# Performance work log

Hardware: AMD Instinct MI355X
Metric: run time of the kernel (lower is better)

## Reference

```python
import jax, jax.numpy as jnp
import numpy as np

C = 64      # n_feats
DG = 8      # deformable groups
K = 3       # kernel size


def _lrelu(v):
    return jnp.where(v >= 0, v, 0.1 * v)


def _conv3x3(v, w, b):
    out = jax.lax.conv_general_dilated(
        v, w, window_strides=(1, 1), padding=((1, 1), (1, 1)),
        dimension_numbers=('NCHW', 'OIHW', 'NCHW'))
    return out + b[None, :, None, None]


def _up2(v):
    # bilinear upsample x2, align_corners=True (separable gather + lerp)
    B, Cc, H, W = v.shape
    def coords(n):
        c = jnp.arange(2 * n, dtype=jnp.float32) * ((n - 1) / (2 * n - 1))
        i0 = jnp.floor(c).astype(jnp.int32)
        i1 = jnp.minimum(i0 + 1, n - 1)
        f = (c - i0).astype(v.dtype)
        return i0, i1, f
    y0, y1, fy = coords(H)
    x0, x1, fx = coords(W)
    t = v[:, :, y0, :] * (1 - fy)[None, None, :, None] + v[:, :, y1, :] * fy[None, None, :, None]
    return t[:, :, :, x0] * (1 - fx)[None, None, None, :] + t[:, :, :, x1] * fx[None, None, None, :]


def _deform_conv(x, offset, mask, w, b):
    # modulated deformable conv (DCNv2), stride=1, pad=1, dil=1
    B, Cc, H, W = x.shape
    K2 = K * K
    cpg = Cc // DG
    off_y = offset[:, :DG * K2].reshape(B, DG, K2, H, W)
    off_x = offset[:, DG * K2:].reshape(B, DG, K2, H, W)
    m = mask.reshape(B, DG, 1, K2, H, W)
    ky, kx = jnp.meshgrid(jnp.arange(K) - 1, jnp.arange(K) - 1, indexing='ij')
    ky = ky.reshape(K2).astype(x.dtype)
    kx = kx.reshape(K2).astype(x.dtype)
    # absolute sampling positions [B, DG, K2, H, W]
    py = off_y + ky[None, None, :, None, None] + jnp.arange(H, dtype=x.dtype)[None, None, None, :, None]
    px = off_x + kx[None, None, :, None, None] + jnp.arange(W, dtype=x.dtype)[None, None, None, None, :]
    y0f = jnp.floor(py)
    x0f = jnp.floor(px)
    wy = py - y0f
    wx = px - x0f
    y0 = y0f.astype(jnp.int32)
    x0 = x0f.astype(jnp.int32)
    xg = x.reshape(B, DG, cpg, H * W)
    def corner(yi, xi, wgt):
        valid = ((yi >= 0) & (yi < H) & (xi >= 0) & (xi < W)).astype(x.dtype)
        yc = jnp.clip(yi, 0, H - 1)
        xc = jnp.clip(xi, 0, W - 1)
        idx = (yc * W + xc).reshape(B, DG, 1, K2 * H * W)
        g = jnp.take_along_axis(xg, jnp.broadcast_to(idx, (B, DG, cpg, K2 * H * W)), axis=3)
        g = g.reshape(B, DG, cpg, K2, H, W)
        return g * (wgt * valid)[:, :, None]
    val = (corner(y0, x0, (1 - wy) * (1 - wx))
           + corner(y0, x0 + 1, (1 - wy) * wx)
           + corner(y0 + 1, x0, wy * (1 - wx))
           + corner(y0 + 1, x0 + 1, wy * wx))
    val = val * m
    wr = w.reshape(Cc, DG, cpg, K2)
    return jnp.einsum('bgckhw,ogck->bohw', val, wr) + b[None, :, None, None]


def setup_inputs() -> dict:
    key = jax.random.key(0)
    ks = jax.random.split(key, 18)
    B, H, W = 2, 128, 128
    def p(k, shape):
        return jax.random.normal(k, shape, jnp.float32) * 0.05
    return {
        'x': jax.random.normal(ks[0], (B, C, H, W), jnp.float32),
        'y': jax.random.normal(ks[1], (B, C, H, W), jnp.float32),
        'prev_offset': jax.random.normal(ks[2], (B, C, H // 2, W // 2), jnp.float32),
        'prev_stage_fea': jax.random.normal(ks[3], (B, C, H // 2, W // 2), jnp.float32),
        'w1': p(ks[4], (C, 2 * C, 3, 3)), 'b1': jnp.zeros((C,), jnp.float32),
        'w2': p(ks[5], (C, 2 * C, 3, 3)), 'b2': jnp.zeros((C,), jnp.float32),
        'w3': p(ks[6], (C, C, 3, 3)), 'b3': jnp.zeros((C,), jnp.float32),
        'w_off': p(ks[7], (DG * 3 * K * K, C, 3, 3)), 'b_off': jnp.zeros((DG * 3 * K * K,), jnp.float32),
        'w_dcn': p(ks[8], (C, C, 3, 3)), 'b_dcn': jnp.zeros((C,), jnp.float32),
        'w_fea': p(ks[9], (C, 2 * C, 3, 3)), 'b_fea': jnp.zeros((C,), jnp.float32),
    }


def reference(x, y, prev_offset, prev_stage_fea,
              w1, b1, w2, b2, w3, b3, w_off, b_off, w_dcn, b_dcn, w_fea, b_fea):
    prev_offset = _up2(prev_offset)
    off = _lrelu(_conv3x3(jnp.concatenate([x, y], axis=1), w1, b1))
    off = _lrelu(_conv3x3(jnp.concatenate([off, prev_offset * 2], axis=1), w2, b2))
    off = _lrelu(_conv3x3(off, w3, b3))
    # DCNv2Pack: offsets/mask predicted from the offset feature
    co = _conv3x3(off, w_off, b_off)
    o1, o2, m = jnp.split(co, 3, axis=1)
    dcn_offset = jnp.concatenate([o1, o2], axis=1)
    m = jax.nn.sigmoid(m)
    fea = _deform_conv(x, dcn_offset, m, w_dcn, b_dcn)
    prev_fea = _up2(prev_stage_fea)
    out = _lrelu(_conv3x3(jnp.concatenate([fea, prev_fea], axis=1), w_fea, b_fea))
    return (off, out)
```

## Files before the change

kernel.cpp:

```cpp
#include <hip/hip_runtime.h>
#include <math.h>

typedef __bf16 bf16x8 __attribute__((ext_vector_type(8)));
typedef float f32x4 __attribute__((ext_vector_type(4)));
typedef unsigned short u16;
typedef __attribute__((address_space(3))) unsigned int lds_u32;
typedef const __attribute__((address_space(1))) unsigned int glb_u32;

__device__ __forceinline__ u16 f2bf(float f) {
    unsigned int u = __builtin_bit_cast(unsigned int, f);
    unsigned int r = (u + 0x7FFFu + ((u >> 16) & 1u)) >> 16;
    return (u16)r;
}
__device__ __forceinline__ float bf2f(u16 u) {
    unsigned int v = ((unsigned int)u) << 16;
    return __builtin_bit_cast(float, v);
}
__device__ __forceinline__ unsigned int pack2(float a, float b) {
    return (unsigned int)f2bf(a) | ((unsigned int)f2bf(b) << 16);
}
__device__ __forceinline__ bf16x8 ld8(const u16* p) {
    uint4 u = *reinterpret_cast<const uint4*>(p);
    return __builtin_bit_cast(bf16x8, u);
}
__device__ __forceinline__ void gload_lds16(const u16* g, u16* l) {
#if __has_builtin(__builtin_amdgcn_global_load_lds)
    __builtin_amdgcn_global_load_lds((glb_u32*)g, (lds_u32*)l, 16, 0, 0);
#else
    *reinterpret_cast<uint4*>(l) = *reinterpret_cast<const uint4*>(g);
#endif
}

__device__ __forceinline__ void dev_zero(u16* base, int nimg, int C, int B, int tid) {
    int idx = B * 256 + tid;
    int c8 = C >> 3;
    int tot = nimg * 516 * c8;
    if (idx >= tot) return;
    int cb = idx % c8;
    int t = idx / c8;
    int pb = t % 516;
    int img = t / 516;
    int y, x;
    if (pb < 130)      { y = 0;        x = pb; }
    else if (pb < 260) { y = 129;      x = pb - 130; }
    else if (pb < 388) { y = pb - 259; x = 0; }
    else               { y = pb - 387; x = 129; }
    u16* d = base + ((size_t)img * 16900 + (size_t)y * 130 + x) * C + cb * 8;
    uint4 z = {0u, 0u, 0u, 0u};
    *reinterpret_cast<uint4*>(d) = z;
}

__device__ __forceinline__ void dev_repack(const float* w, u16* dst,
                                           int Cout, int Cin, int mode, int B, int tid) {
    int idx = B * 256 + tid;
    int total = Cout * Cin * 9;
    if (idx >= total) return;
    int kk = idx % 9;
    int t = idx / 9;
    int ci = t % Cin;
    int o = t / Cin;
    u16 v = f2bf(w[idx]);
    size_t d;
    if (mode == 0) d = (size_t)o * (9 * Cin) + kk * Cin + ci;
    else           d = (size_t)o * 576 + (ci >> 3) * 72 + kk * 8 + (ci & 7);
    dst[d] = v;
}

__device__ __forceinline__ void dev_to_nhwc(const float* src, u16* dst,
                                            int c0, int Ctot, int B, int tid) {
    int idx = B * 256 + tid;
    int pix = idx & 16383, b = idx >> 14;
    int y = pix >> 7, x = pix & 127;
    const float* s = src + (size_t)b * 64 * 16384 + pix;
    u16* d = dst + (((size_t)b * 16900) + (size_t)(y + 1) * 130 + (x + 1)) * Ctot + c0;
#pragma unroll
    for (int q = 0; q < 8; ++q) {
        float v0 = s[(size_t)(q * 8 + 0) * 16384], v1 = s[(size_t)(q * 8 + 1) * 16384];
        float v2 = s[(size_t)(q * 8 + 2) * 16384], v3 = s[(size_t)(q * 8 + 3) * 16384];
        float v4 = s[(size_t)(q * 8 + 4) * 16384], v5 = s[(size_t)(q * 8 + 5) * 16384];
        float v6 = s[(size_t)(q * 8 + 6) * 16384], v7 = s[(size_t)(q * 8 + 7) * 16384];
        uint4 u;
        u.x = pack2(v0, v1); u.y = pack2(v2, v3); u.z = pack2(v4, v5); u.w = pack2(v6, v7);
        *reinterpret_cast<uint4*>(d + q * 8) = u;
    }
}

__device__ __forceinline__ void dev_up2(const float* src, u16* dst,
                                        int c0, int Ctot, float scale, int B, int tid) {
    int idx = B * 256 + tid;
    int pix = idx & 16383, b = idx >> 14;
    int y = pix >> 7, x = pix & 127;
    const float f = 63.0f / 127.0f;
    float cy = y * f, cx = x * f;
    float y0f = floorf(cy), x0f = floorf(cx);
    int y0 = (int)y0f, x0 = (int)x0f;
    int y1 = min(y0 + 1, 63), x1 = min(x0 + 1, 63);
    float fy = cy - y0f, fx = cx - x0f;
    float w00 = (1.f - fy) * (1.f - fx) * scale, w01 = (1.f - fy) * fx * scale;
    float w10 = fy * (1.f - fx) * scale, w11 = fy * fx * scale;
    int i00 = y0 * 64 + x0, i01 = y0 * 64 + x1, i10 = y1 * 64 + x0, i11 = y1 * 64 + x1;
    const float* s = src + (size_t)b * 64 * 4096;
    u16* d = dst + (((size_t)b * 16900) + (size_t)(y + 1) * 130 + (x + 1)) * Ctot + c0;
#pragma unroll
    for (int q = 0; q < 8; ++q) {
        float v[8];
#pragma unroll
        for (int c = 0; c < 8; ++c) {
            const float* p = s + (size_t)(q * 8 + c) * 4096;
            v[c] = w00 * p[i00] + w01 * p[i01] + w10 * p[i10] + w11 * p[i11];
        }
        uint4 u;
        u.x = pack2(v[0], v[1]); u.y = pack2(v[2], v[3]);
        u.z = pack2(v[4], v[5]); u.w = pack2(v[6], v[7]);
        *reinterpret_cast<uint4*>(d + q * 8) = u;
    }
}

__global__ __launch_bounds__(256) void preproc(
    const float* __restrict__ x, const float* __restrict__ y,
    const float* __restrict__ prev_off, const float* __restrict__ prev_fea,
    const float* __restrict__ w1, const float* __restrict__ w2,
    const float* __restrict__ w3, const float* __restrict__ w_off,
    const float* __restrict__ w_dcn, const float* __restrict__ w_fea,
    u16* __restrict__ T1, u16* __restrict__ T3, u16* __restrict__ T9,
    u16* __restrict__ T4,
    u16* __restrict__ wq1, u16* __restrict__ wq2, u16* __restrict__ wq3,
    u16* __restrict__ wqo, u16* __restrict__ wqd, u16* __restrict__ wqf) {
    int B = blockIdx.x, tid = threadIdx.x;
    if (B < 129) { dev_zero(T1, 4, 128, B, tid); return; }  B -= 129;
    if (B < 65)  { dev_zero(T9, 2, 128, B, tid); return; }  B -= 65;
    if (B < 65)  { dev_zero(T4, 4, 64, B, tid); return; }   B -= 65;
    if (B < 288) { dev_repack(w1, wq1, 64, 128, 0, B, tid); return; }   B -= 288;
    if (B < 288) { dev_repack(w2, wq2, 64, 128, 0, B, tid); return; }   B -= 288;
    if (B < 144) { dev_repack(w3, wq3, 64, 64, 0, B, tid); return; }    B -= 144;
    if (B < 486) { dev_repack(w_off, wqo, 216, 64, 0, B, tid); return; } B -= 486;
    if (B < 144) { dev_repack(w_dcn, wqd, 64, 64, 1, B, tid); return; } B -= 144;
    if (B < 288) { dev_repack(w_fea, wqf, 64, 128, 0, B, tid); return; } B -= 288;
    if (B < 128) { dev_to_nhwc(x, T1, 0, 128, B, tid); return; }        B -= 128;
    if (B < 128) { dev_to_nhwc(y, T1, 64, 128, B, tid); return; }       B -= 128;
    if (B < 128) { dev_up2(prev_off, T3, 64, 128, 2.0f, B, tid); return; } B -= 128;
    dev_up2(prev_fea, T9, 64, 128, 1.0f, B, tid);
}

template<int CIN, int WAVES, int KSPLIT, int ACTM, bool NHWC_OUT, bool OUT_PAD, int NCHW_MODE>
__global__ __launch_bounds__(WAVES * 64) void conv_tile(
    const u16* __restrict__ in, const u16* __restrict__ wgt,
    const float* __restrict__ bias,
    u16* __restrict__ outN, int c0, int Ctot,
    void* __restrict__ outC, int Cout) {
    constexpr int T = WAVES * 64;
    constexpr int PXW = WAVES / KSPLIT;
    constexpr int BPR = 4 / PXW;
    constexpr int KCH = CIN / KSPLIT;
    constexpr int CSTEPS = KCH / 32;
    constexpr int MSK = (CIN == 128) ? 15 : 7;
    constexpr int RSH = (CIN == 128) ? 8 : 7;
    __shared__ __align__(16) u16 As[2][64 * CIN];

    const int tid = threadIdx.x;
    const int lane = tid & 63;
    const int wv = tid >> 6;
    const int kslice = wv % KSPLIT;
    const int pxc = wv / KSPLIT;
    const int gx = blockIdx.x;
    const int xh = gx % BPR;
    const int y = (gx / BPR) & 127;
    const int b = gx / (BPR * 128);
    const int mblk = blockIdx.y << 6;
    const int n0 = lane & 15;
    const int kq = lane >> 4;
    const int xbase = xh * (PXW * 32) + pxc * 32;

    const u16* inB = in + (size_t)b * 16900 * CIN;

#define STAGE(ss, bf) {                                                        \
        _Pragma("unroll")                                                      \
        for (int i_ = 0; i_ < (8 * CIN) / T; ++i_) {                           \
            int L_ = (i_ * T + tid) * 16;                                      \
            int row_ = L_ >> RSH;                                              \
            int c16_ = (L_ >> 4) & MSK;                                        \
            int sc_ = c16_ ^ (row_ & MSK);                                     \
            const u16* src_ = wgt + (size_t)(mblk + row_) * (9 * CIN)          \
                              + (ss) * CIN + sc_ * 8;                          \
            gload_lds16(src_, &As[bf][L_ >> 1]);                               \
        }                                                                      \
    }

    f32x4 acc[4][2] = {};

    STAGE(0, 0)
    __syncthreads();

    for (int s = 0; s < 9; ++s) {
        const int buf = s & 1;
        if (s < 8) STAGE(s + 1, buf ^ 1)

        const int dy = s / 3, dx = s - dy * 3;
        const u16* brow = inB + ((size_t)(y + dy) * 130 + (xbase + n0 + dx)) * CIN
                          + kq * 8;
        const u16* ab = &As[buf][0];
#pragma unroll
        for (int c = 0; c < CSTEPS; ++c) {
            const int kch = kslice * KCH + c * 32;
            bf16x8 b0 = ld8(brow + kch);
            bf16x8 b1 = ld8(brow + 16 * CIN + kch);
            const int colb = (((kch >> 3) + kq) ^ (n0 & MSK)) * 8;
            bf16x8 a0 = ld8(ab + (0 * 16 + n0) * CIN + colb);
            bf16x8 a1 = ld8(ab + (1 * 16 + n0) * CIN + colb);
            bf16x8 a2 = ld8(ab + (2 * 16 + n0) * CIN + colb);
            bf16x8 a3 = ld8(ab + (3 * 16 + n0) * CIN + colb);
            acc[0][0] = __builtin_amdgcn_mfma_f32_16x16x32_bf16(a0, b0, acc[0][0], 0, 0, 0);
            acc[0][1] = __builtin_amdgcn_mfma_f32_16x16x32_bf16(a0, b1, acc[0][1], 0, 0, 0);
            acc[1][0] = __builtin_amdgcn_mfma_f32_16x16x32_bf16(a1, b0, acc[1][0], 0, 0, 0);
            acc[1][1] = __builtin_amdgcn_mfma_f32_16x16x32_bf16(a1, b1, acc[1][1], 0, 0, 0);
            acc[2][0] = __builtin_amdgcn_mfma_f32_16x16x32_bf16(a2, b0, acc[2][0], 0, 0, 0);
            acc[2][1] = __builtin_amdgcn_mfma_f32_16x16x32_bf16(a2, b1, acc[2][1], 0, 0, 0);
            acc[3][0] = __builtin_amdgcn_mfma_f32_16x16x32_bf16(a3, b0, acc[3][0], 0, 0, 0);
            acc[3][1] = __builtin_amdgcn_mfma_f32_16x16x32_bf16(a3, b1, acc[3][1], 0, 0, 0);
        }
        __syncthreads();
    }
#undef STAGE

    if (KSPLIT == 2) {
        float* red = (float*)(&As[0][0]);
        if (kslice == 1) {
#pragma unroll
            for (int mt = 0; mt < 4; ++mt)
#pragma unroll
                for (int nt = 0; nt < 2; ++nt)
                    *reinterpret_cast<f32x4*>(
                        &red[((pxc * 8) + mt * 2 + nt) * 256 + lane * 4]) = acc[mt][nt];
        }
        __syncthreads();
        if (kslice == 1) return;
#pragma unroll
        for (int mt = 0; mt < 4; ++mt)
#pragma unroll
            for (int nt = 0; nt < 2; ++nt)
                acc[mt][nt] += *reinterpret_cast<const f32x4*>(
                    &red[((pxc * 8) + mt * 2 + nt) * 256 + lane * 4]);
    }

#pragma unroll
    for (int mt = 0; mt < 4; ++mt) {
        const int mbase = mblk + mt * 16 + kq * 4;
        float bs0 = 0.f, bs1 = 0.f, bs2 = 0.f, bs3 = 0.f;
        if (mbase < Cout) {
            bs0 = bias[mbase]; bs1 = bias[mbase + 1];
            bs2 = bias[mbase + 2]; bs3 = bias[mbase + 3];
        }
#pragma unroll
        for (int nt = 0; nt < 2; ++nt) {
            const int xx = xbase + nt * 16 + n0;
            float v0 = acc[mt][nt][0] + bs0, v1 = acc[mt][nt][1] + bs1;
            float v2 = acc[mt][nt][2] + bs2, v3 = acc[mt][nt][3] + bs3;
            if (ACTM == 1) {
                v0 = (v0 >= 0.f) ? v0 : 0.1f * v0;
                v1 = (v1 >= 0.f) ? v1 : 0.1f * v1;
                v2 = (v2 >= 0.f) ? v2 : 0.1f * v2;
                v3 = (v3 >= 0.f) ? v3 : 0.1f * v3;
            } else if (ACTM == 2) {
                if (mbase >= 144) {
                    v0 = 1.f / (1.f + expf(-v0));
                    v1 = 1.f / (1.f + expf(-v1));
                    v2 = 1.f / (1.f + expf(-v2));
                    v3 = 1.f / (1.f + expf(-v3));
                }
            }
            if (NHWC_OUT && mbase < Cout) {
                size_t pix = OUT_PAD ? ((size_t)(y + 1) * 130 + xx + 1)
                                     : ((size_t)y * 128 + xx);
                size_t off = ((size_t)b * (OUT_PAD ? 16900 : 16384) + pix) * Ctot + c0 + mbase;
                uint2 u;
                u.x = pack2(v0, v1); u.y = pack2(v2, v3);
                *reinterpret_cast<uint2*>(outN + off) = u;
            }
            if (NCHW_MODE == 1 && mbase < Cout) {
                float* oc = (float*)outC;
                size_t o = ((size_t)(b * Cout + mbase)) * 16384 + (size_t)y * 128 + xx;
                oc[o] = v0; oc[o + 16384] = v1;
                oc[o + 2 * 16384] = v2; oc[o + 3 * 16384] = v3;
            }
            if (NCHW_MODE == 2 && mbase < Cout) {
                u16* oc = (u16*)outC;
                size_t o = ((size_t)(b * Cout + mbase)) * 16384 + (size_t)y * 128 + xx;
                oc[o] = f2bf(v0); oc[o + 16384] = f2bf(v1);
                oc[o + 2 * 16384] = f2bf(v2); oc[o + 3 * 16384] = f2bf(v3);
            }
        }
    }
}

__global__ __launch_bounds__(256, 2) void dcn_fused(
    const u16* __restrict__ xn, const u16* __restrict__ co,
    const u16* __restrict__ wgt, const float* __restrict__ bias,
    u16* __restrict__ outN) {
    __shared__ u16 lw[64 * 584];
    {
        int t = threadIdx.x;
        int o = t >> 2, chunk = t & 3;
        const u16* src = wgt + o * 576 + chunk * 144;
        u16* dst = lw + o * 584 + chunk * 144;
#pragma unroll
        for (int i = 0; i < 18; ++i)
            *reinterpret_cast<uint4*>(dst + i * 8) =
                *reinterpret_cast<const uint4*>(src + i * 8);
    }
    __syncthreads();

    const int lane = threadIdx.x & 63;
    const int wv = threadIdx.x >> 6;
    const int half = blockIdx.x & 1;
    const int y = (blockIdx.x >> 1) & 127;
    const int b = blockIdx.x >> 8;
    const int n0 = lane & 15;
    const int kq = lane >> 4;
    const int xx = half * 64 + wv * 16 + n0;
    const int p = y * 128 + xx;

    const u16* cob = co + (size_t)b * 216 * 16384 + p;
    const u16* xb = xn + (size_t)b * 16900 * 128;

    float offy[18], offx[18], mvv[18];
#pragma unroll
    for (int cs = 0; cs < 18; ++cs) {
        int gk8 = cs * 4 + kq;
        offy[cs] = bf2f(cob[(size_t)gk8 * 16384]);
        offx[cs] = bf2f(cob[(size_t)(72 + gk8) * 16384]);
        mvv[cs]  = bf2f(cob[(size_t)(144 + gk8) * 16384]);
    }

    f32x4 acc[4] = {};
    float w00[2], w01[2], w10[2], w11[2];
    uint4 q00[2], q01[2], q10[2], q11[2];

#define DCN_GL(cs, st) {                                                       \
        int gk8_ = (cs) * 4 + kq;                                              \
        int g_ = (gk8_ * 57) >> 9;                                             \
        int kk_ = gk8_ - 9 * g_;                                               \
        int ky_ = (kk_ * 11) >> 5;                                             \
        int kx_ = kk_ - 3 * ky_;                                               \
        float py_ = offy[cs] + (float)(ky_ - 1) + (float)y;                    \
        float px_ = offx[cs] + (float)(kx_ - 1) + (float)xx;                   \
        float y0f_ = floorf(py_), x0f_ = floorf(px_);                          \
        float wy_ = py_ - y0f_, wx_ = px_ - x0f_;                              \
        int y0_ = (int)y0f_, x0_ = (int)x0f_, y1_ = y0_ + 1, x1_ = x0_ + 1;    \
        float m00_ = ((unsigned)y0_ < 128u && (unsigned)x0_ < 128u) ? 1.f : 0.f; \
        float m01_ = ((unsigned)y0_ < 128u && (unsigned)x1_ < 128u) ? 1.f : 0.f; \
        float m10_ = ((unsigned)y1_ < 128u && (unsigned)x0_ < 128u) ? 1.f : 0.f; \
        float m11_ = ((unsigned)y1_ < 128u && (unsigned)x1_ < 128u) ? 1.f : 0.f; \
        float mv_ = mvv[cs];                                                   \
        w00[st] = (1.f - wy_) * (1.f - wx_) * m00_ * mv_;                      \
        w01[st] = (1.f - wy_) * wx_ * m01_ * mv_;                              \
        w10[st] = wy_ * (1.f - wx_) * m10_ * mv_;                              \
        w11[st] = wy_ * wx_ * m11_ * mv_;                                      \
        int y0c_ = min(max(y0_, 0), 127), y1c_ = min(max(y1_, 0), 127);        \
        int x0c_ = min(max(x0_, 0), 127), x1c_ = min(max(x1_, 0), 127);        \
        const u16* xg_ = xb + g_ * 8;                                          \
        q00[st] = *reinterpret_cast<const uint4*>(xg_ + ((size_t)(y0c_ + 1) * 130 + x0c_ + 1) * 128); \
        q01[st] = *reinterpret_cast<const uint4*>(xg_ + ((size_t)(y0c_ + 1) * 130 + x1c_ + 1) * 128); \
        q10[st] = *reinterpret_cast<const uint4*>(xg_ + ((size_t)(y1c_ + 1) * 130 + x0c_ + 1) * 128); \
        q11[st] = *reinterpret_cast<const uint4*>(xg_ + ((size_t)(y1c_ + 1) * 130 + x1c_ + 1) * 128); \
    }

#define DCN_GU(cs, st) {                                                       \
        const unsigned int* a00_ = &q00[st].x; const unsigned int* a01_ = &q01[st].x; \
        const unsigned int* a10_ = &q10[st].x; const unsigned int* a11_ = &q11[st].x; \
        float r_[8];                                                           \
        _Pragma("unroll")                                                      \
        for (int c = 0; c < 8; ++c) {                                          \
            unsigned int u00_ = a00_[c >> 1], u01_ = a01_[c >> 1];             \
            unsigned int u10_ = a10_[c >> 1], u11_ = a11_[c >> 1];             \
            int sh_ = (c & 1) * 16;                                            \
            float f00_ = bf2f((u16)(u00_ >> sh_)), f01_ = bf2f((u16)(u01_ >> sh_)); \
            float f10_ = bf2f((u16)(u10_ >> sh_)), f11_ = bf2f((u16)(u11_ >> sh_)); \
            r_[c] = w00[st] * f00_ + w01[st] * f01_ + w10[st] * f10_ + w11[st] * f11_; \
        }                                                                      \
        uint4 bu_;                                                             \
        bu_.x = pack2(r_[0], r_[1]); bu_.y = pack2(r_[2], r_[3]);              \
        bu_.z = pack2(r_[4], r_[5]); bu_.w = pack2(r_[6], r_[7]);              \
        bf16x8 bfrag_ = __builtin_bit_cast(bf16x8, bu_);                       \
        const int kcol_ = (cs) * 32 + kq * 8;                                  \
        bf16x8 a0_ = ld8(lw + (size_t)(0 * 16 + n0) * 584 + kcol_);            \
        bf16x8 a1_ = ld8(lw + (size_t)(1 * 16 + n0) * 584 + kcol_);            \
        bf16x8 a2_ = ld8(lw + (size_t)(2 * 16 + n0) * 584 + kcol_);            \
        bf16x8 a3_ = ld8(lw + (size_t)(3 * 16 + n0) * 584 + kcol_);            \
        acc[0] = __builtin_amdgcn_mfma_f32_16x16x32_bf16(a0_, bfrag_, acc[0], 0, 0, 0); \
        acc[1] = __builtin_amdgcn_mfma_f32_16x16x32_bf16(a1_, bfrag_, acc[1], 0, 0, 0); \
        acc[2] = __builtin_amdgcn_mfma_f32_16x16x32_bf16(a2_, bfrag_, acc[2], 0, 0, 0); \
        acc[3] = __builtin_amdgcn_mfma_f32_16x16x32_bf16(a3_, bfrag_, acc[3], 0, 0, 0); \
    }

    DCN_GL(0, 0)
    DCN_GL(1, 1)
#pragma unroll
    for (int cs = 0; cs < 18; cs += 2) {
        DCN_GU(cs, 0)
        if (cs + 2 < 18) DCN_GL(cs + 2, 0)
        DCN_GU(cs + 1, 1)
        if (cs + 3 < 18) DCN_GL(cs + 3, 1)
    }
#undef DCN_GL
#undef DCN_GU

#pragma unroll
    for (int mt = 0; mt < 4; ++mt) {
        const int mbase = mt * 16 + kq * 4;
        float v0 = acc[mt][0] + bias[mbase];
        float v1 = acc[mt][1] + bias[mbase + 1];
        float v2 = acc[mt][2] + bias[mbase + 2];
        float v3 = acc[mt][3] + bias[mbase + 3];
        size_t off = ((size_t)b * 16900 + (size_t)(y + 1) * 130 + (xx + 1)) * 128 + mbase;
        uint2 u;
        u.x = pack2(v0, v1); u.y = pack2(v2, v3);
        *reinterpret_cast<uint2*>(outN + off) = u;
    }
}

#define T1_OFF 0u
#define T3_OFF 8652800u
#define T9_OFF 17305600u
#define T4_OFF 25958400u
#define T5_OFF 30284800u
#define T6_OFF 34611200u
#define W1_OFF 48766976u
#define W2_OFF 48914432u
#define W3_OFF 49061888u
#define WF_OFF 49135616u
#define WO_OFF 49283072u
#define WD_OFF 49577984u

extern "C" void kernel_launch(void* const* d_in, const int* in_sizes, int n_in,
                              void* d_out, int out_size, void* d_ws, size_t ws_size,
                              hipStream_t stream) {
    const float* x        = (const float*)d_in[0];
    const float* y        = (const float*)d_in[1];
    const float* prev_off = (const float*)d_in[2];
    const float* prev_fea = (const float*)d_in[3];
    const float* w1 = (const float*)d_in[4];  const float* b1 = (const float*)d_in[5];
    const float* w2 = (const float*)d_in[6];  const float* b2 = (const float*)d_in[7];
    const float* w3 = (const float*)d_in[8];  const float* b3 = (const float*)d_in[9];
    const float* w_off = (const float*)d_in[10]; const float* b_off = (const float*)d_in[11];
    const float* w_dcn = (const float*)d_in[12]; const float* b_dcn = (const float*)d_in[13];
    const float* w_fea = (const float*)d_in[14]; const float* b_fea = (const float*)d_in[15];

    float* out_off = (float*)d_out;
    float* out_out = (float*)d_out + (size_t)2 * 64 * 16384;

    char* ws = (char*)d_ws;
    u16* T1 = (u16*)(ws + T1_OFF);
    u16* T3 = (u16*)(ws + T3_OFF);
    u16* T9 = (u16*)(ws + T9_OFF);
    u16* T4 = (u16*)(ws + T4_OFF);
    u16* T5 = (u16*)(ws + T5_OFF);
    u16* T6 = (u16*)(ws + T6_OFF);
    u16* wq1 = (u16*)(ws + W1_OFF);
    u16* wq2 = (u16*)(ws + W2_OFF);
    u16* wq3 = (u16*)(ws + W3_OFF);
    u16* wqf = (u16*)(ws + WF_OFF);
    u16* wqo = (u16*)(ws + WO_OFF);
    u16* wqd = (u16*)(ws + WD_OFF);

    preproc<<<dim3(2409), dim3(256), 0, stream>>>(
        x, y, prev_off, prev_fea, w1, w2, w3, w_off, w_dcn, w_fea,
        T1, T3, T9, T4, wq1, wq2, wq3, wqo, wqd, wqf);

    conv_tile<128, 4, 2, 1, true, true, 0><<<dim3(512, 1), dim3(256), 0, stream>>>(
        T1, wq1, b1, T3, 0, 128, nullptr, 64);
    conv_tile<128, 4, 2, 1, true, true, 0><<<dim3(512, 1), dim3(256), 0, stream>>>(
        T3, wq2, b2, T4, 0, 64, nullptr, 64);
    conv_tile<64, 2, 1, 1, true, true, 1><<<dim3(512, 1), dim3(128), 0, stream>>>(
        T4, wq3, b3, T5, 0, 64, out_off, 64);
    conv_tile<64, 2, 1, 2, false, false, 2><<<dim3(512, 4), dim3(128), 0, stream>>>(
        T5, wqo, b_off, nullptr, 0, 0, T6, 216);
    dcn_fused<<<dim3(512), dim3(256), 0, stream>>>(T1, T6, wqd, b_dcn, T9);
    conv_tile<128, 4, 2, 1, false, false, 1><<<dim3(512, 1), dim3(256), 0, stream>>>(
        T9, wqf, b_fea, nullptr, 0, 0, out_out, 64);
}
```

Before: 142.1 us.

## Stage all nine weight taps into LDS once instead of double-buffering per tap

```diff
diff --git a/kernel.cpp b/kernel.cpp
--- a/kernel.cpp
+++ b/kernel.cpp
@@ -154,8 +154,10 @@
     constexpr int KCH = CIN / KSPLIT;
     constexpr int CSTEPS = KCH / 32;
     constexpr int MSK = (CIN == 128) ? 15 : 7;
-    constexpr int RSH = (CIN == 128) ? 8 : 7;
-    __shared__ __align__(16) u16 As[2][64 * CIN];
+    constexpr int SPR = CIN / 8;
+    constexpr int SPS = 64 * SPR;
+    constexpr int NSTG = 72 * CIN / T;
+    extern __shared__ __align__(16) u16 As[];
 
     const int tid = threadIdx.x;
     const int lane = tid & 63;
@@ -173,38 +175,33 @@
 
     const u16* inB = in + (size_t)b * 16900 * CIN;
 
-#define STAGE(ss, bf) {                                                        \
-        _Pragma("unroll")                                                      \
-        for (int i_ = 0; i_ < (8 * CIN) / T; ++i_) {                           \
-            int L_ = (i_ * T + tid) * 16;                                      \
-            int row_ = L_ >> RSH;                                              \
-            int c16_ = (L_ >> 4) & MSK;                                        \
-            int sc_ = c16_ ^ (row_ & MSK);                                     \
-            const u16* src_ = wgt + (size_t)(mblk + row_) * (9 * CIN)          \
-                              + (ss) * CIN + sc_ * 8;                          \
-            gload_lds16(src_, &As[bf][L_ >> 1]);                               \
-        }                                                                      \
-    }
+#pragma unroll
+    for (int i = 0; i < NSTG; ++i) {
+        int ls = i * T + tid;
+        int s = ls / SPS;
+        int w = ls - s * SPS;
+        int r = w / SPR;
+        int c16 = w - r * SPR;
+        int sc = c16 ^ (r & MSK);
+        const u16* src = wgt + (size_t)(mblk + r) * (9 * CIN) + s * CIN + sc * 8;
+        gload_lds16(src, &As[(size_t)ls * 8]);
+    }
+    __syncthreads();
 
     f32x4 acc[4][2] = {};
 
-    STAGE(0, 0)
-    __syncthreads();
-
+#pragma unroll
     for (int s = 0; s < 9; ++s) {
-        const int buf = s & 1;
-        if (s < 8) STAGE(s + 1, buf ^ 1)
-
         const int dy = s / 3, dx = s - dy * 3;
         const u16* brow = inB + ((size_t)(y + dy) * 130 + (xbase + n0 + dx)) * CIN
                           + kq * 8;
-        const u16* ab = &As[buf][0];
+        const u16* ab = As + (size_t)s * (64 * CIN);
 #pragma unroll
         for (int c = 0; c < CSTEPS; ++c) {
             const int kch = kslice * KCH + c * 32;
             bf16x8 b0 = ld8(brow + kch);
             bf16x8 b1 = ld8(brow + 16 * CIN + kch);
-            const int colb = (((kch >> 3) + kq) ^ (n0 & MSK)) * 8;
+            const int colb = ((((kch >> 3) + kq)) ^ (n0 & MSK)) * 8;
             bf16x8 a0 = ld8(ab + (0 * 16 + n0) * CIN + colb);
             bf16x8 a1 = ld8(ab + (1 * 16 + n0) * CIN + colb);
             bf16x8 a2 = ld8(ab + (2 * 16 + n0) * CIN + colb);
@@ -218,12 +215,11 @@
             acc[3][0] = __builtin_amdgcn_mfma_f32_16x16x32_bf16(a3, b0, acc[3][0], 0, 0, 0);
             acc[3][1] = __builtin_amdgcn_mfma_f32_16x16x32_bf16(a3, b1, acc[3][1], 0, 0, 0);
         }
+    }
+
+    if (KSPLIT == 2) {
+        float* red = (float*)As;
         __syncthreads();
-    }
-#undef STAGE
-
-    if (KSPLIT == 2) {
-        float* red = (float*)(&As[0][0]);
         if (kslice == 1) {
 #pragma unroll
             for (int mt = 0; mt < 4; ++mt)
@@ -462,19 +458,28 @@
     u16* wqo = (u16*)(ws + WO_OFF);
     u16* wqd = (u16*)(ws + WD_OFF);
 
+    auto kA = (const void*)conv_tile<128, 4, 2, 1, true, true, 0>;
+    auto kF = (const void*)conv_tile<128, 4, 2, 1, false, false, 1>;
+    auto k3 = (const void*)conv_tile<64, 2, 1, 1, true, true, 1>;
+    auto kO = (const void*)conv_tile<64, 2, 1, 2, false, false, 2>;
+    hipFuncSetAttribute(kA, hipFuncAttributeMaxDynamicSharedMemorySize, 147456);
+    hipFuncSetAttribute(kF, hipFuncAttributeMaxDynamicSharedMemorySize, 147456);
+    hipFuncSetAttribute(k3, hipFuncAttributeMaxDynamicSharedMemorySize, 73728);
+    hipFuncSetAttribute(kO, hipFuncAttributeMaxDynamicSharedMemorySize, 73728);
+
     preproc<<<dim3(2409), dim3(256), 0, stream>>>(
         x, y, prev_off, prev_fea, w1, w2, w3, w_off, w_dcn, w_fea,
         T1, T3, T9, T4, wq1, wq2, wq3, wqo, wqd, wqf);
 
-    conv_tile<128, 4, 2, 1, true, true, 0><<<dim3(512, 1), dim3(256), 0, stream>>>(
+    conv_tile<128, 4, 2, 1, true, true, 0><<<dim3(512, 1), dim3(256), 147456, stream>>>(
         T1, wq1, b1, T3, 0, 128, nullptr, 64);
-    conv_tile<128, 4, 2, 1, true, true, 0><<<dim3(512, 1), dim3(256), 0, stream>>>(
+    conv_tile<128, 4, 2, 1, true, true, 0><<<dim3(512, 1), dim3(256), 147456, stream>>>(
         T3, wq2, b2, T4, 0, 64, nullptr, 64);
-    conv_tile<64, 2, 1, 1, true, true, 1><<<dim3(512, 1), dim3(128), 0, stream>>>(
+    conv_tile<64, 2, 1, 1, true, true, 1><<<dim3(512, 1), dim3(128), 73728, stream>>>(
         T4, wq3, b3, T5, 0, 64, out_off, 64);
-    conv_tile<64, 2, 1, 2, false, false, 2><<<dim3(512, 4), dim3(128), 0, stream>>>(
+    conv_tile<64, 2, 1, 2, false, false, 2><<<dim3(512, 4), dim3(128), 73728, stream>>>(
         T5, wqo, b_off, nullptr, 0, 0, T6, 216);
     dcn_fused<<<dim3(512), dim3(256), 0, stream>>>(T1, T6, wqd, b_dcn, T9);
-    conv_tile<128, 4, 2, 1, false, false, 1><<<dim3(512, 1), dim3(256), 0, stream>>>(
+    conv_tile<128, 4, 2, 1, false, false, 1><<<dim3(512, 1), dim3(256), 147456, stream>>>(
         T9, wqf, b_fea, nullptr, 0, 0, out_out, 64);
 }
```

Result: slower. 150.3 us (+5.7%).
